# Kernel tuning notes

Hardware: AMD Instinct MI355X
Metric: run time of the kernel (lower is better)

The kernel has to match this reference:

```python
import jax, jax.numpy as jnp
import numpy as np

NUM_ITERATIONS = 3


def squash(s):
    # s: [..., out_channels]; norm over last axis (matches torch squash on squeezed tensor)
    norm = jnp.linalg.norm(s, axis=-1, keepdims=True)
    return (norm ** 2 / (1.0 + norm ** 2)) * (s / norm)


def setup_inputs() -> dict:
    key = jax.random.key(0)
    k1, k2 = jax.random.split(key)
    B, R, C, O, I = 256, 192, 96, 16, 20
    x = jax.random.normal(k1, (B, R, I), dtype=jnp.float32)
    W = jax.random.normal(k2, (R, C, O, I), dtype=jnp.float32)
    return {"x": x, "W": W}


def reference(x, W):
    # u_hat[b,r,c,o] = W[r,c,o,i] @ x[b,r,i]  (torch: matmul(W, x[i]) per batch element)
    u_hat = jnp.einsum('rcoi,bri->brco', W, x)  # [B,R,C,O]
    R, C = W.shape[0], W.shape[1]
    b_ij = jnp.zeros((R, C), dtype=x.dtype)  # shared across batch (torch b_ij is [1,R,C,1])
    v_j = None
    for it in range(NUM_ITERATIONS):
        c_ij = jax.nn.softmax(b_ij, axis=0)                 # softmax over routes (dim=1 in torch)
        s_j = jnp.einsum('rc,brco->bco', c_ij, u_hat)        # weighted sum over routes
        v_j = squash(s_j)                                    # [B,C,O]
        if it < NUM_ITERATIONS - 1:
            # agreement: <u_hat, v_j> averaged over batch (torch mean(dim=0))
            a_ij = jnp.einsum('brco,bco->rc', u_hat, v_j) / x.shape[0]
            b_ij = b_ij + a_ij
    return v_j  # [B, num_capsules, out_channels] (torch returns trailing singleton [B,C,O,1])
```

## Files before the change

### kernel.cpp

```cpp
#include <hip/hip_runtime.h>


#define R_ 192
#define C_ 96
#define O_ 16
#define I_ 20
#define B_ 256
#define K1 3840
#define N_ 1536
#define ZSPLIT 20
#define STILE 393216

typedef unsigned short u16;
typedef __attribute__((ext_vector_type(8))) short short8;
typedef __attribute__((ext_vector_type(4))) float floatx4;

__device__ inline float bf2f(u16 h) {
  union { unsigned int u; float f; } x; x.u = ((unsigned int)h) << 16; return x.f;
}
__device__ inline u16 f2bf(float f) {
  union { float f; unsigned int u; } x; x.f = f;
  unsigned int r = x.u + 0x7FFFu + ((x.u >> 16) & 1u);
  return (u16)(r >> 16);
}
__device__ inline unsigned int pack2(float a, float b) {
  return (unsigned int)f2bf(a) | ((unsigned int)f2bf(b) << 16);
}

__global__ void k_prep(const float* __restrict__ W, const float* __restrict__ X,
                       u16* __restrict__ WtT, u16* __restrict__ Xk,
                       u16* __restrict__ xT, float* __restrict__ bij) {
  int bid = blockIdx.x;
  if (bid < 23040) {
    int t = bid * 256 + threadIdx.x;
    int n = t / K1, k = t - n * K1;
    int c = n >> 4, o = n & 15;
    int r = k / I_, i = k - r * I_;
    WtT[t] = f2bf(W[(((r * C_ + c) * O_ + o) * I_) + i]);
  } else if (bid < 23280) {
    __shared__ u16 tile[64][72];
    int idx = bid - 23040;
    int kb = (idx % 60) << 6, bb = (idx / 60) << 6;
    int brow = threadIdx.x >> 4;
    int kq = (threadIdx.x & 15) << 2;
    #pragma unroll
    for (int p = 0; p < 4; ++p) {
      int bl = p * 16 + brow;
      float4 v = *(const float4*)(X + (size_t)(bb + bl) * K1 + kb + kq);
      ushort4 h;
      h.x = f2bf(v.x); h.y = f2bf(v.y); h.z = f2bf(v.z); h.w = f2bf(v.w);
      *(ushort4*)(Xk + (size_t)(bb + bl) * K1 + kb + kq) = h;
      tile[kq + 0][bl] = h.x;
      tile[kq + 1][bl] = h.y;
      tile[kq + 2][bl] = h.z;
      tile[kq + 3][bl] = h.w;
    }
    __syncthreads();
    int kr = threadIdx.x >> 3;
    int bq = (threadIdx.x & 7) << 3;
    #pragma unroll
    for (int q = 0; q < 2; ++q) {
      int kl = q * 32 + kr;
      *(uint4*)(xT + (size_t)(kb + kl) * B_ + bb + bq) = *(const uint4*)&tile[kl][bq];
    }
  } else {
    int t = (bid - 23280) * 256 + threadIdx.x;
    bij[t] = 0.0f;
  }
}

__device__ inline uint4 scale_b8(uint4 raw, int kg, const float* smrow) {
  int r0 = kg / I_;
  int bnd = (r0 + 1) * I_ - kg;
  float s0 = smrow[r0];
  float s1 = smrow[(r0 + 1 < R_) ? r0 + 1 : R_ - 1];
  union { uint4 q; u16 h[8]; } u; u.q = raw;
  #pragma unroll
  for (int j = 0; j < 8; ++j)
    u.h[j] = f2bf(bf2f(u.h[j]) * ((j < bnd) ? s0 : s1));
  return u.q;
}

__global__ __launch_bounds__(256) void gemm1(
    const u16* __restrict__ A, const u16* __restrict__ Bt,
    const float* __restrict__ bij, u16* __restrict__ P,
    int kChunk, int kIters) {
  __shared__ u16 As[2][128 * 32];
  __shared__ u16 Bs[2][128 * 32];
  __shared__ float sm[8][192];
  int tid = threadIdx.x;
  {
    int cg = tid >> 5, lr = tid & 31;
    int c = (blockIdx.y << 3) + cg;
    float e[6]; float mx = -1e30f;
    #pragma unroll
    for (int j = 0; j < 6; ++j) {
      e[j] = bij[(lr + (j << 5)) * C_ + c];
      mx = fmaxf(mx, e[j]);
    }
    #pragma unroll
    for (int off = 16; off > 0; off >>= 1) mx = fmaxf(mx, __shfl_xor(mx, off));
    float sum = 0.f;
    #pragma unroll
    for (int j = 0; j < 6; ++j) { e[j] = expf(e[j] - mx); sum += e[j]; }
    #pragma unroll
    for (int off = 16; off > 0; off >>= 1) sum += __shfl_xor(sum, off);
    float inv = 1.0f / sum;
    #pragma unroll
    for (int j = 0; j < 6; ++j) sm[cg][lr + (j << 5)] = e[j] * inv;
  }

  long m0 = (long)blockIdx.x * 128, n0 = (long)blockIdx.y * 128;
  int k0 = blockIdx.z * kChunk;
  const u16* Ab = A + m0 * K1 + k0;
  const u16* Bb = Bt + n0 * K1 + k0;
  int srow = tid >> 2;
  int scol = (tid & 3) << 3;
  int w = tid >> 6, lane = tid & 63;
  int wm = (w >> 1) << 6, wn = (w & 1) << 6;
  int quad = lane >> 4, lrow = lane & 15;
  int cl0 = srow >> 4;
  floatx4 acc[4][4];
  #pragma unroll
  for (int a = 0; a < 4; ++a)
    #pragma unroll
    for (int b = 0; b < 4; ++b) acc[a][b] = (floatx4){0.f, 0.f, 0.f, 0.f};

  uint4 a0 = *(const uint4*)(Ab + (long)srow * K1 + scol);
  uint4 a1 = *(const uint4*)(Ab + (long)(srow + 64) * K1 + scol);
  uint4 b0 = *(const uint4*)(Bb + (long)srow * K1 + scol);
  uint4 b1 = *(const uint4*)(Bb + (long)(srow + 64) * K1 + scol);
  __syncthreads();

  int p = 0;
  for (int kt = 0; kt < kIters; ++kt) {
    int kg = k0 + (kt << 5) + scol;
    ((uint4*)As[p])[tid] = a0;
    ((uint4*)As[p])[tid + 256] = a1;
    ((uint4*)Bs[p])[tid] = scale_b8(b0, kg, &sm[cl0][0]);
    ((uint4*)Bs[p])[tid + 256] = scale_b8(b1, kg, &sm[cl0 + 4][0]);
    __syncthreads();
    if (kt + 1 < kIters) {
      int kk = (kt + 1) << 5;
      a0 = *(const uint4*)(Ab + (long)srow * K1 + kk + scol);
      a1 = *(const uint4*)(Ab + (long)(srow + 64) * K1 + kk + scol);
      b0 = *(const uint4*)(Bb + (long)srow * K1 + kk + scol);
      b1 = *(const uint4*)(Bb + (long)(srow + 64) * K1 + kk + scol);
    }
    short8 af[4], bfr[4];
    #pragma unroll
    for (int ms = 0; ms < 4; ++ms)
      af[ms] = *(const short8*)&As[p][(wm + ms * 16 + lrow) * 32 + (quad << 3)];
    #pragma unroll
    for (int ns = 0; ns < 4; ++ns)
      bfr[ns] = *(const short8*)&Bs[p][(wn + ns * 16 + lrow) * 32 + (quad << 3)];
    #pragma unroll
    for (int ms = 0; ms < 4; ++ms)
      #pragma unroll
      for (int ns = 0; ns < 4; ++ns)
        acc[ms][ns] = __builtin_amdgcn_mfma_f32_16x16x32_bf16(
            af[ms], bfr[ns], acc[ms][ns], 0, 0, 0);
    p ^= 1;
  }
  size_t zb = (size_t)blockIdx.z * (size_t)STILE;
  #pragma unroll
  for (int ms = 0; ms < 4; ++ms)
    #pragma unroll
    for (int ns = 0; ns < 4; ++ns) {
      int b = (int)m0 + wm + ms * 16 + (quad << 2);
      int n = (int)n0 + wn + ns * 16 + lrow;
      uint2 pk;
      pk.x = pack2(acc[ms][ns][0], acc[ms][ns][1]);
      pk.y = pack2(acc[ms][ns][2], acc[ms][ns][3]);
      *(uint2*)&P[zb + (size_t)n * B_ + b] = pk;
    }
}

__global__ void k_redsq(const u16* __restrict__ P, float* __restrict__ out,
                        u16* __restrict__ vT, int last) {
  __shared__ float nsq_l[4][128];
  int c = blockIdx.x, bh = blockIdx.y;
  int lane = threadIdx.x & 63, og = threadIdx.x >> 6;
  int bi = (lane << 1);
  int b = (bh << 7) + bi;
  float acc[4][2];
  #pragma unroll
  for (int oo = 0; oo < 4; ++oo) { acc[oo][0] = 0.f; acc[oo][1] = 0.f; }
  for (int z = 0; z < ZSPLIT; ++z) {
    size_t base = (size_t)z * STILE + (size_t)((c << 4) + (og << 2)) * B_ + b;
    #pragma unroll
    for (int oo = 0; oo < 4; ++oo) {
      unsigned int u = *(const unsigned int*)&P[base + (size_t)oo * B_];
      acc[oo][0] += bf2f((u16)(u & 0xffff));
      acc[oo][1] += bf2f((u16)(u >> 16));
    }
  }
  float q0 = 0.f, q1 = 0.f;
  #pragma unroll
  for (int oo = 0; oo < 4; ++oo) {
    q0 += acc[oo][0] * acc[oo][0];
    q1 += acc[oo][1] * acc[oo][1];
  }
  nsq_l[og][bi] = q0;
  nsq_l[og][bi + 1] = q1;
  __syncthreads();
  float n0 = nsq_l[0][bi] + nsq_l[1][bi] + nsq_l[2][bi] + nsq_l[3][bi];
  float n1 = nsq_l[0][bi + 1] + nsq_l[1][bi + 1] + nsq_l[2][bi + 1] + nsq_l[3][bi + 1];
  float f0 = n0 / ((1.0f + n0) * sqrtf(n0));
  float f1 = n1 / ((1.0f + n1) * sqrtf(n1));
  #pragma unroll
  for (int oo = 0; oo < 4; ++oo) { acc[oo][0] *= f0; acc[oo][1] *= f1; }
  if (last) {
    float4 v0 = (float4){acc[0][0], acc[1][0], acc[2][0], acc[3][0]};
    float4 v1 = (float4){acc[0][1], acc[1][1], acc[2][1], acc[3][1]};
    *(float4*)(out + (size_t)b * N_ + (c << 4) + (og << 2)) = v0;
    *(float4*)(out + (size_t)(b + 1) * N_ + (c << 4) + (og << 2)) = v1;
  } else {
    #pragma unroll
    for (int oo = 0; oo < 4; ++oo)
      *(unsigned int*)&vT[(size_t)((c << 4) + (og << 2) + oo) * B_ + b] =
          pack2(acc[oo][0], acc[oo][1]);
  }
}

__global__ __launch_bounds__(256) void gemm2_agree(
    const u16* __restrict__ A, const u16* __restrict__ Bt,
    const u16* __restrict__ WtT, float* __restrict__ bij) {
  const int K = 256;
  __shared__ u16 As[2][128 * 32];
  __shared__ u16 Bs[2][128 * 32];
  int tid = threadIdx.x;
  long m0 = (long)blockIdx.x * 128, n0 = (long)blockIdx.y * 128;
  int k0 = blockIdx.z << 7;
  const u16* Ab = A + m0 * K + k0;
  const u16* Bb = Bt + n0 * K + k0;
  int srow = tid >> 2;
  int scol = (tid & 3) << 3;
  int w = tid >> 6, lane = tid & 63;
  int wm = (w >> 1) << 6, wn = (w & 1) << 6;
  int quad = lane >> 4, lrow = lane & 15;
  floatx4 acc[4][4];
  #pragma unroll
  for (int a = 0; a < 4; ++a)
    #pragma unroll
    for (int b = 0; b < 4; ++b) acc[a][b] = (floatx4){0.f, 0.f, 0.f, 0.f};

  uint4 a0 = *(const uint4*)(Ab + (long)srow * K + scol);
  uint4 a1 = *(const uint4*)(Ab + (long)(srow + 64) * K + scol);
  uint4 b0 = *(const uint4*)(Bb + (long)srow * K + scol);
  uint4 b1 = *(const uint4*)(Bb + (long)(srow + 64) * K + scol);

  int p = 0;
  #pragma unroll
  for (int kt = 0; kt < 4; ++kt) {
    ((uint4*)As[p])[tid] = a0;
    ((uint4*)As[p])[tid + 256] = a1;
    ((uint4*)Bs[p])[tid] = b0;
    ((uint4*)Bs[p])[tid + 256] = b1;
    __syncthreads();
    if (kt + 1 < 4) {
      int kk = (kt + 1) << 5;
      a0 = *(const uint4*)(Ab + (long)srow * K + kk + scol);
      a1 = *(const uint4*)(Ab + (long)(srow + 64) * K + kk + scol);
      b0 = *(const uint4*)(Bb + (long)srow * K + kk + scol);
      b1 = *(const uint4*)(Bb + (long)(srow + 64) * K + kk + scol);
    }
    short8 af[4], bfr[4];
    #pragma unroll
    for (int ms = 0; ms < 4; ++ms)
      af[ms] = *(const short8*)&As[p][(wm + ms * 16 + lrow) * 32 + (quad << 3)];
    #pragma unroll
    for (int ns = 0; ns < 4; ++ns)
      bfr[ns] = *(const short8*)&Bs[p][(wn + ns * 16 + lrow) * 32 + (quad << 3)];
    #pragma unroll
    for (int ms = 0; ms < 4; ++ms)
      #pragma unroll
      for (int ns = 0; ns < 4; ++ns)
        acc[ms][ns] = __builtin_amdgcn_mfma_f32_16x16x32_bf16(
            af[ms], bfr[ns], acc[ms][ns], 0, 0, 0);
    p ^= 1;
  }
  #pragma unroll
  for (int ms = 0; ms < 4; ++ms) {
    int rowbase = (int)m0 + wm + ms * 16;
    int r_lo = rowbase / I_;
    int r_hi = (rowbase + 15) / I_;
    int bnd = (r_lo + 1) * I_;
    int rowl = rowbase + (quad << 2);
    #pragma unroll
    for (int ns = 0; ns < 4; ++ns) {
      int col = (int)n0 + wn + ns * 16 + lrow;
      uint2 wv = *(const uint2*)&WtT[(size_t)col * K1 + rowl];
      u16 h[4];
      h[0] = (u16)(wv.x & 0xffff); h[1] = (u16)(wv.x >> 16);
      h[2] = (u16)(wv.y & 0xffff); h[3] = (u16)(wv.y >> 16);
      float p0 = 0.f, p1 = 0.f;
      #pragma unroll
      for (int e = 0; e < 4; ++e) {
        float pr = acc[ms][ns][e] * bf2f(h[e]);
        if (rowl + e < bnd) p0 += pr; else p1 += pr;
      }
      #pragma unroll
      for (int off = 32; off > 0; off >>= 1) {
        p0 += __shfl_xor(p0, off);
        p1 += __shfl_xor(p1, off);
      }
      if (lane == 0) {
        int c = col >> 4;
        atomicAdd(&bij[r_lo * C_ + c], p0 * (1.0f / 256.0f));
        atomicAdd(&bij[r_hi * C_ + c], p1 * (1.0f / 256.0f));
      }
    }
  }
}

extern "C" void kernel_launch(void* const* d_in, const int* in_sizes, int n_in,
                              void* d_out, int out_size, void* d_ws, size_t ws_size,
                              hipStream_t stream) {
  const float* X = (const float*)d_in[0];
  const float* W = (const float*)d_in[1];
  float* out = (float*)d_out;
  char* ws = (char*)d_ws;
  u16*  WtT = (u16*)(ws);
  u16*  Xk  = (u16*)(ws + 11796480);
  u16*  xT  = (u16*)(ws + 13762560);
  u16*  vT  = (u16*)(ws + 15728640);
  u16*  Pb  = (u16*)(ws + 16515072);
  float* bij = (float*)(ws + 32243712);

  k_prep<<<23352, 256, 0, stream>>>(W, X, WtT, Xk, xT, bij);

  for (int it = 0; it < 3; ++it) {
    gemm1<<<dim3(2, 12, ZSPLIT), 256, 0, stream>>>(Xk, WtT, bij, Pb, 192, 6);
    k_redsq<<<dim3(96, 2), 256, 0, stream>>>(Pb, out, vT, it == 2);
    if (it < 2)
      gemm2_agree<<<dim3(30, 12, 2), 256, 0, stream>>>(xT, vT, WtT, bij);
  }
}
```

Before: 176.0 us.

## Precompute softmax in separate kernel, shrink gemm1 M-tile, skip scaling on first iteration

The routing softmax moves out of every gemm1 block into a small k_cij kernel that runs once per iteration, and gemm1 now just loads the precomputed coefficients. On the first iteration, where the coefficients are uniform, the B-operand scaling is skipped and a 1/192 factor is applied in the reduction kernel instead. The gemm1 M tile is halved from 128 to 64 rows, which doubles the grid and is meant to raise occupancy. The cost is less register-level reuse per block and one extra small launch per iteration.

```diff
diff --git a/kernel.cpp b/kernel.cpp
--- a/kernel.cpp
+++ b/kernel.cpp
@@ -69,6 +69,22 @@
   }
 }
 
+__global__ void k_cij(const float* __restrict__ bij, float* __restrict__ cij) {
+  int c = blockIdx.x, l = threadIdx.x;
+  float v0 = bij[l * C_ + c], v1 = bij[(l + 64) * C_ + c], v2 = bij[(l + 128) * C_ + c];
+  float m = fmaxf(v0, fmaxf(v1, v2));
+  #pragma unroll
+  for (int off = 32; off > 0; off >>= 1) m = fmaxf(m, __shfl_xor(m, off));
+  float e0 = expf(v0 - m), e1 = expf(v1 - m), e2 = expf(v2 - m);
+  float s = e0 + e1 + e2;
+  #pragma unroll
+  for (int off = 32; off > 0; off >>= 1) s += __shfl_xor(s, off);
+  float inv = 1.0f / s;
+  cij[c * R_ + l] = e0 * inv;
+  cij[c * R_ + l + 64] = e1 * inv;
+  cij[c * R_ + l + 128] = e2 * inv;
+}
+
 __device__ inline uint4 scale_b8(uint4 raw, int kg, const float* smrow) {
   int r0 = kg / I_;
   int bnd = (r0 + 1) * I_ - kg;
@@ -83,81 +99,70 @@
 
 __global__ __launch_bounds__(256) void gemm1(
     const u16* __restrict__ A, const u16* __restrict__ Bt,
-    const float* __restrict__ bij, u16* __restrict__ P,
-    int kChunk, int kIters) {
-  __shared__ u16 As[2][128 * 32];
+    const float* __restrict__ cij, u16* __restrict__ P, int doScale) {
+  __shared__ u16 As[2][64 * 32];
   __shared__ u16 Bs[2][128 * 32];
   __shared__ float sm[8][192];
   int tid = threadIdx.x;
-  {
-    int cg = tid >> 5, lr = tid & 31;
-    int c = (blockIdx.y << 3) + cg;
-    float e[6]; float mx = -1e30f;
+  if (doScale) {
     #pragma unroll
     for (int j = 0; j < 6; ++j) {
-      e[j] = bij[(lr + (j << 5)) * C_ + c];
-      mx = fmaxf(mx, e[j]);
-    }
-    #pragma unroll
-    for (int off = 16; off > 0; off >>= 1) mx = fmaxf(mx, __shfl_xor(mx, off));
-    float sum = 0.f;
-    #pragma unroll
-    for (int j = 0; j < 6; ++j) { e[j] = expf(e[j] - mx); sum += e[j]; }
-    #pragma unroll
-    for (int off = 16; off > 0; off >>= 1) sum += __shfl_xor(sum, off);
-    float inv = 1.0f / sum;
-    #pragma unroll
-    for (int j = 0; j < 6; ++j) sm[cg][lr + (j << 5)] = e[j] * inv;
-  }
-
-  long m0 = (long)blockIdx.x * 128, n0 = (long)blockIdx.y * 128;
-  int k0 = blockIdx.z * kChunk;
-  const u16* Ab = A + m0 * K1 + k0;
-  const u16* Bb = Bt + n0 * K1 + k0;
+      int idx = tid + j * 256;
+      int cl = idx / R_, r = idx - cl * R_;
+      sm[cl][r] = cij[((blockIdx.y << 3) + cl) * R_ + r];
+    }
+  }
+
+  int m0 = blockIdx.x << 6, n0 = blockIdx.y << 7;
+  int k0 = blockIdx.z * 192;
+  const u16* Ab = A + (size_t)m0 * K1 + k0;
+  const u16* Bb = Bt + (size_t)n0 * K1 + k0;
   int srow = tid >> 2;
   int scol = (tid & 3) << 3;
   int w = tid >> 6, lane = tid & 63;
-  int wm = (w >> 1) << 6, wn = (w & 1) << 6;
+  int wn = w << 5;
   int quad = lane >> 4, lrow = lane & 15;
   int cl0 = srow >> 4;
-  floatx4 acc[4][4];
+  floatx4 acc[4][2];
   #pragma unroll
   for (int a = 0; a < 4; ++a)
     #pragma unroll
-    for (int b = 0; b < 4; ++b) acc[a][b] = (floatx4){0.f, 0.f, 0.f, 0.f};
-
-  uint4 a0 = *(const uint4*)(Ab + (long)srow * K1 + scol);
-  uint4 a1 = *(const uint4*)(Ab + (long)(srow + 64) * K1 + scol);
-  uint4 b0 = *(const uint4*)(Bb + (long)srow * K1 + scol);
-  uint4 b1 = *(const uint4*)(Bb + (long)(srow + 64) * K1 + scol);
+    for (int b = 0; b < 2; ++b) acc[a][b] = (floatx4){0.f, 0.f, 0.f, 0.f};
+
+  uint4 a0 = *(const uint4*)(Ab + (size_t)srow * K1 + scol);
+  uint4 b0 = *(const uint4*)(Bb + (size_t)srow * K1 + scol);
+  uint4 b1 = *(const uint4*)(Bb + (size_t)(srow + 64) * K1 + scol);
   __syncthreads();
 
   int p = 0;
-  for (int kt = 0; kt < kIters; ++kt) {
-    int kg = k0 + (kt << 5) + scol;
+  for (int kt = 0; kt < 6; ++kt) {
     ((uint4*)As[p])[tid] = a0;
-    ((uint4*)As[p])[tid + 256] = a1;
-    ((uint4*)Bs[p])[tid] = scale_b8(b0, kg, &sm[cl0][0]);
-    ((uint4*)Bs[p])[tid + 256] = scale_b8(b1, kg, &sm[cl0 + 4][0]);
+    if (doScale) {
+      int kg = k0 + (kt << 5) + scol;
+      ((uint4*)Bs[p])[tid] = scale_b8(b0, kg, &sm[cl0][0]);
+      ((uint4*)Bs[p])[tid + 256] = scale_b8(b1, kg, &sm[cl0 + 4][0]);
+    } else {
+      ((uint4*)Bs[p])[tid] = b0;
+      ((uint4*)Bs[p])[tid + 256] = b1;
+    }
     __syncthreads();
-    if (kt + 1 < kIters) {
+    if (kt + 1 < 6) {
       int kk = (kt + 1) << 5;
-      a0 = *(const uint4*)(Ab + (long)srow * K1 + kk + scol);
-      a1 = *(const uint4*)(Ab + (long)(srow + 64) * K1 + kk + scol);
-      b0 = *(const uint4*)(Bb + (long)srow * K1 + kk + scol);
-      b1 = *(const uint4*)(Bb + (long)(srow + 64) * K1 + kk + scol);
-    }
-    short8 af[4], bfr[4];
+      a0 = *(const uint4*)(Ab + (size_t)srow * K1 + kk + scol);
+      b0 = *(const uint4*)(Bb + (size_t)srow * K1 + kk + scol);
+      b1 = *(const uint4*)(Bb + (size_t)(srow + 64) * K1 + kk + scol);
+    }
+    short8 af[4], bfr[2];
     #pragma unroll
     for (int ms = 0; ms < 4; ++ms)
-      af[ms] = *(const short8*)&As[p][(wm + ms * 16 + lrow) * 32 + (quad << 3)];
-    #pragma unroll
-    for (int ns = 0; ns < 4; ++ns)
+      af[ms] = *(const short8*)&As[p][(ms * 16 + lrow) * 32 + (quad << 3)];
+    #pragma unroll
+    for (int ns = 0; ns < 2; ++ns)
       bfr[ns] = *(const short8*)&Bs[p][(wn + ns * 16 + lrow) * 32 + (quad << 3)];
     #pragma unroll
     for (int ms = 0; ms < 4; ++ms)
       #pragma unroll
-      for (int ns = 0; ns < 4; ++ns)
+      for (int ns = 0; ns < 2; ++ns)
         acc[ms][ns] = __builtin_amdgcn_mfma_f32_16x16x32_bf16(
             af[ms], bfr[ns], acc[ms][ns], 0, 0, 0);
     p ^= 1;
@@ -166,9 +171,9 @@
   #pragma unroll
   for (int ms = 0; ms < 4; ++ms)
     #pragma unroll
-    for (int ns = 0; ns < 4; ++ns) {
-      int b = (int)m0 + wm + ms * 16 + (quad << 2);
-      int n = (int)n0 + wn + ns * 16 + lrow;
+    for (int ns = 0; ns < 2; ++ns) {
+      int b = m0 + ms * 16 + (quad << 2);
+      int n = n0 + wn + ns * 16 + lrow;
       uint2 pk;
       pk.x = pack2(acc[ms][ns][0], acc[ms][ns][1]);
       pk.y = pack2(acc[ms][ns][2], acc[ms][ns][3]);
@@ -177,7 +182,7 @@
 }
 
 __global__ void k_redsq(const u16* __restrict__ P, float* __restrict__ out,
-                        u16* __restrict__ vT, int last) {
+                        u16* __restrict__ vT, float preScale, int last) {
   __shared__ float nsq_l[4][128];
   int c = blockIdx.x, bh = blockIdx.y;
   int lane = threadIdx.x & 63, og = threadIdx.x >> 6;
@@ -195,6 +200,8 @@
       acc[oo][1] += bf2f((u16)(u >> 16));
     }
   }
+  #pragma unroll
+  for (int oo = 0; oo < 4; ++oo) { acc[oo][0] *= preScale; acc[oo][1] *= preScale; }
   float q0 = 0.f, q1 = 0.f;
   #pragma unroll
   for (int oo = 0; oo < 4; ++oo) {
@@ -327,13 +334,17 @@
   u16*  vT  = (u16*)(ws + 15728640);
   u16*  Pb  = (u16*)(ws + 16515072);
   float* bij = (float*)(ws + 32243712);
+  float* cij = (float*)(ws + 32317440);
 
   k_prep<<<23352, 256, 0, stream>>>(W, X, WtT, Xk, xT, bij);
 
   for (int it = 0; it < 3; ++it) {
-    gemm1<<<dim3(2, 12, ZSPLIT), 256, 0, stream>>>(Xk, WtT, bij, Pb, 192, 6);
-    k_redsq<<<dim3(96, 2), 256, 0, stream>>>(Pb, out, vT, it == 2);
-    if (it < 2)
+    gemm1<<<dim3(4, 12, ZSPLIT), 256, 0, stream>>>(Xk, WtT, cij, Pb, it > 0);
+    k_redsq<<<dim3(96, 2), 256, 0, stream>>>(
+        Pb, out, vT, it == 0 ? (1.0f / 192.0f) : 1.0f, it == 2);
+    if (it < 2) {
       gemm2_agree<<<dim3(30, 12, 2), 256, 0, stream>>>(xT, vT, WtT, bij);
-  }
-}
+      k_cij<<<96, 64, 0, stream>>>(bij, cij);
+    }
+  }
+}
```

New measurement: 182.6 us. 3.7% more time.

## Use direct global-to-LDS loads in GEMMs, vectorize weight conversion, transpose routing logits

Applied to the files above, without the earlier changes.

The GEMM tile loads now go straight from global memory into LDS with global_load_lds, skipping the register staging. This covers the A operand in gemm1 and both operands in gemm2. The weight bf16 conversion in k_prep now handles four elements per thread with a vectorized store, and the bij zeroing writes float4. The routing logits change to a [C][R] layout so gemm1's softmax reads are contiguous, and the kernel loop bounds are hard-coded. The async LDS writes rely on the existing barriers for ordering, and a missing wait on the async loads could create a race.

```diff
diff --git a/kernel.cpp b/kernel.cpp
--- a/kernel.cpp
+++ b/kernel.cpp
@@ -26,20 +26,33 @@
 __device__ inline unsigned int pack2(float a, float b) {
   return (unsigned int)f2bf(a) | ((unsigned int)f2bf(b) << 16);
 }
+__device__ inline void async16(const u16* g, u16* l) {
+  __builtin_amdgcn_global_load_lds(
+      (__attribute__((address_space(1))) void*)(unsigned long long)g,
+      (__attribute__((address_space(3))) void*)(unsigned int)(unsigned long long)l,
+      16, 0, 0);
+}
 
 __global__ void k_prep(const float* __restrict__ W, const float* __restrict__ X,
                        u16* __restrict__ WtT, u16* __restrict__ Xk,
                        u16* __restrict__ xT, float* __restrict__ bij) {
   int bid = blockIdx.x;
-  if (bid < 23040) {
-    int t = bid * 256 + threadIdx.x;
+  if (bid < 5760) {
+    int t = (bid * 256 + threadIdx.x) << 2;
     int n = t / K1, k = t - n * K1;
     int c = n >> 4, o = n & 15;
-    int r = k / I_, i = k - r * I_;
-    WtT[t] = f2bf(W[(((r * C_ + c) * O_ + o) * I_) + i]);
-  } else if (bid < 23280) {
+    const float* Wn = W + (size_t)(c * O_ + o) * I_;
+    u16 h[4];
+    #pragma unroll
+    for (int e = 0; e < 4; ++e) {
+      int ke = k + e, r = ke / I_, i = ke - r * I_;
+      h[e] = f2bf(Wn[(size_t)r * (C_ * O_ * I_) + i]);
+    }
+    ushort4 o4; o4.x = h[0]; o4.y = h[1]; o4.z = h[2]; o4.w = h[3];
+    *(ushort4*)&WtT[t] = o4;
+  } else if (bid < 6000) {
     __shared__ u16 tile[64][72];
-    int idx = bid - 23040;
+    int idx = bid - 5760;
     int kb = (idx % 60) << 6, bb = (idx / 60) << 6;
     int brow = threadIdx.x >> 4;
     int kq = (threadIdx.x & 15) << 2;
@@ -64,8 +77,8 @@
       *(uint4*)(xT + (size_t)(kb + kl) * B_ + bb + bq) = *(const uint4*)&tile[kl][bq];
     }
   } else {
-    int t = (bid - 23280) * 256 + threadIdx.x;
-    bij[t] = 0.0f;
+    int t = ((bid - 6000) * 256 + threadIdx.x) << 2;
+    if (t < R_ * C_) *(float4*)&bij[t] = (float4){0.f, 0.f, 0.f, 0.f};
   }
 }
 
@@ -83,8 +96,7 @@
 
 __global__ __launch_bounds__(256) void gemm1(
     const u16* __restrict__ A, const u16* __restrict__ Bt,
-    const float* __restrict__ bij, u16* __restrict__ P,
-    int kChunk, int kIters) {
+    const float* __restrict__ bij, u16* __restrict__ P) {
   __shared__ u16 As[2][128 * 32];
   __shared__ u16 Bs[2][128 * 32];
   __shared__ float sm[8][192];
@@ -95,7 +107,7 @@
     float e[6]; float mx = -1e30f;
     #pragma unroll
     for (int j = 0; j < 6; ++j) {
-      e[j] = bij[(lr + (j << 5)) * C_ + c];
+      e[j] = bij[c * R_ + lr + (j << 5)];
       mx = fmaxf(mx, e[j]);
     }
     #pragma unroll
@@ -111,7 +123,7 @@
   }
 
   long m0 = (long)blockIdx.x * 128, n0 = (long)blockIdx.y * 128;
-  int k0 = blockIdx.z * kChunk;
+  int k0 = blockIdx.z * 192;
   const u16* Ab = A + m0 * K1 + k0;
   const u16* Bb = Bt + n0 * K1 + k0;
   int srow = tid >> 2;
@@ -120,30 +132,31 @@
   int wm = (w >> 1) << 6, wn = (w & 1) << 6;
   int quad = lane >> 4, lrow = lane & 15;
   int cl0 = srow >> 4;
+  int wb = w << 9;
+  const u16* Ag0 = Ab + (long)srow * K1 + scol;
+  const u16* Ag1 = Ab + (long)(srow + 64) * K1 + scol;
   floatx4 acc[4][4];
   #pragma unroll
   for (int a = 0; a < 4; ++a)
     #pragma unroll
     for (int b = 0; b < 4; ++b) acc[a][b] = (floatx4){0.f, 0.f, 0.f, 0.f};
 
-  uint4 a0 = *(const uint4*)(Ab + (long)srow * K1 + scol);
-  uint4 a1 = *(const uint4*)(Ab + (long)(srow + 64) * K1 + scol);
+  async16(Ag0, &As[0][wb]);
+  async16(Ag1, &As[0][2048 + wb]);
   uint4 b0 = *(const uint4*)(Bb + (long)srow * K1 + scol);
   uint4 b1 = *(const uint4*)(Bb + (long)(srow + 64) * K1 + scol);
   __syncthreads();
 
   int p = 0;
-  for (int kt = 0; kt < kIters; ++kt) {
+  for (int kt = 0; kt < 6; ++kt) {
     int kg = k0 + (kt << 5) + scol;
-    ((uint4*)As[p])[tid] = a0;
-    ((uint4*)As[p])[tid + 256] = a1;
     ((uint4*)Bs[p])[tid] = scale_b8(b0, kg, &sm[cl0][0]);
     ((uint4*)Bs[p])[tid + 256] = scale_b8(b1, kg, &sm[cl0 + 4][0]);
     __syncthreads();
-    if (kt + 1 < kIters) {
+    if (kt + 1 < 6) {
       int kk = (kt + 1) << 5;
-      a0 = *(const uint4*)(Ab + (long)srow * K1 + kk + scol);
-      a1 = *(const uint4*)(Ab + (long)(srow + 64) * K1 + kk + scol);
+      async16(Ag0 + kk, &As[p ^ 1][wb]);
+      async16(Ag1 + kk, &As[p ^ 1][2048 + wb]);
       b0 = *(const uint4*)(Bb + (long)srow * K1 + kk + scol);
       b1 = *(const uint4*)(Bb + (long)(srow + 64) * K1 + kk + scol);
     }
@@ -239,31 +252,32 @@
   int w = tid >> 6, lane = tid & 63;
   int wm = (w >> 1) << 6, wn = (w & 1) << 6;
   int quad = lane >> 4, lrow = lane & 15;
+  int wb = w << 9;
+  const u16* Ag0 = Ab + (long)srow * K + scol;
+  const u16* Ag1 = Ab + (long)(srow + 64) * K + scol;
+  const u16* Bg0 = Bb + (long)srow * K + scol;
+  const u16* Bg1 = Bb + (long)(srow + 64) * K + scol;
   floatx4 acc[4][4];
   #pragma unroll
   for (int a = 0; a < 4; ++a)
     #pragma unroll
     for (int b = 0; b < 4; ++b) acc[a][b] = (floatx4){0.f, 0.f, 0.f, 0.f};
 
-  uint4 a0 = *(const uint4*)(Ab + (long)srow * K + scol);
-  uint4 a1 = *(const uint4*)(Ab + (long)(srow + 64) * K + scol);
-  uint4 b0 = *(const uint4*)(Bb + (long)srow * K + scol);
-  uint4 b1 = *(const uint4*)(Bb + (long)(srow + 64) * K + scol);
+  async16(Ag0, &As[0][wb]);
+  async16(Ag1, &As[0][2048 + wb]);
+  async16(Bg0, &Bs[0][wb]);
+  async16(Bg1, &Bs[0][2048 + wb]);
 
   int p = 0;
   #pragma unroll
   for (int kt = 0; kt < 4; ++kt) {
-    ((uint4*)As[p])[tid] = a0;
-    ((uint4*)As[p])[tid + 256] = a1;
-    ((uint4*)Bs[p])[tid] = b0;
-    ((uint4*)Bs[p])[tid + 256] = b1;
     __syncthreads();
     if (kt + 1 < 4) {
       int kk = (kt + 1) << 5;
-      a0 = *(const uint4*)(Ab + (long)srow * K + kk + scol);
-      a1 = *(const uint4*)(Ab + (long)(srow + 64) * K + kk + scol);
-      b0 = *(const uint4*)(Bb + (long)srow * K + kk + scol);
-      b1 = *(const uint4*)(Bb + (long)(srow + 64) * K + kk + scol);
+      async16(Ag0 + kk, &As[p ^ 1][wb]);
+      async16(Ag1 + kk, &As[p ^ 1][2048 + wb]);
+      async16(Bg0 + kk, &Bs[p ^ 1][wb]);
+      async16(Bg1 + kk, &Bs[p ^ 1][2048 + wb]);
     }
     short8 af[4], bfr[4];
     #pragma unroll
@@ -307,8 +321,8 @@
       }
       if (lane == 0) {
         int c = col >> 4;
-        atomicAdd(&bij[r_lo * C_ + c], p0 * (1.0f / 256.0f));
-        atomicAdd(&bij[r_hi * C_ + c], p1 * (1.0f / 256.0f));
+        atomicAdd(&bij[c * R_ + r_lo], p0 * (1.0f / 256.0f));
+        atomicAdd(&bij[c * R_ + r_hi], p1 * (1.0f / 256.0f));
       }
     }
   }
@@ -328,10 +342,10 @@
   u16*  Pb  = (u16*)(ws + 16515072);
   float* bij = (float*)(ws + 32243712);
 
-  k_prep<<<23352, 256, 0, stream>>>(W, X, WtT, Xk, xT, bij);
+  k_prep<<<6018, 256, 0, stream>>>(W, X, WtT, Xk, xT, bij);
 
   for (int it = 0; it < 3; ++it) {
-    gemm1<<<dim3(2, 12, ZSPLIT), 256, 0, stream>>>(Xk, WtT, bij, Pb, 192, 6);
+    gemm1<<<dim3(2, 12, ZSPLIT), 256, 0, stream>>>(Xk, WtT, bij, Pb);
     k_redsq<<<dim3(96, 2), 256, 0, stream>>>(Pb, out, vT, it == 2);
     if (it < 2)
       gemm2_agree<<<dim3(30, 12, 2), 256, 0, stream>>>(xT, vT, WtT, bij);
```

After: 167.5 us. 4.8% less time.
